# Optimization experiments

Measured on AMD Instinct MI355X. Metric: run time of the kernel, lower is better.

## Reference

```python
import jax, jax.numpy as jnp
import numpy as np

N_NODES = 10000
N_EDGES = 640000

def _gcn_conv(h, src, dst, W, b):
    # PyG GCNConv: add self-loops, symmetric deg normalization, then linear.
    # Apply linear first (same math, smaller messages).
    n = h.shape[0]
    h = h @ W  # [N, out]
    loops = jnp.arange(n)
    s = jnp.concatenate([src, loops])
    d = jnp.concatenate([dst, loops])
    deg = jax.ops.segment_sum(jnp.ones_like(s, dtype=h.dtype), d, num_segments=n)
    dinv = jnp.where(deg > 0, deg ** -0.5, 0.0)
    norm = dinv[s] * dinv[d]  # [E+N]
    msgs = h[s] * norm[:, None]
    out = jax.ops.segment_sum(msgs, d, num_segments=n)
    return out + b


def setup_inputs() -> dict:
    key = jax.random.key(0)
    ks = jax.random.split(key, 6)
    x = jax.random.normal(ks[0], (N_NODES, N_NODES), dtype=jnp.float32)
    edge_index = jax.random.randint(ks[1], (2, N_EDGES), 0, N_NODES, dtype=jnp.int64)
    emb = jax.random.normal(ks[2], (N_NODES, 256), dtype=jnp.float32)
    W1 = jax.random.normal(ks[3], (256, 64), dtype=jnp.float32) * (1.0 / np.sqrt(256))
    b1 = jnp.zeros((64,), dtype=jnp.float32)
    W2 = jax.random.normal(ks[4], (64, 32), dtype=jnp.float32) * (1.0 / np.sqrt(64))
    b2 = jnp.zeros((32,), dtype=jnp.float32)
    dec_W = jax.random.normal(ks[5], (32, 16), dtype=jnp.float32) * (1.0 / np.sqrt(32))
    return {"x": x, "edge_index": edge_index, "emb": emb, "W1": W1, "b1": b1,
            "W2": W2, "b2": b2, "dec_W": dec_W}


def reference(x, edge_index, emb, W1, b1, W2, b2, dec_W):
    src, dst = edge_index[0], edge_index[1]
    h = jax.nn.relu(x @ emb)                      # [N, 256]
    h = jax.nn.relu(_gcn_conv(h, src, dst, W1, b1))  # [N, 64]
    h = jax.nn.relu(_gcn_conv(h, src, dst, W2, b2))  # [N, 32]
    logits = h @ dec_W                            # multi-class inner-product decoder
    return logits
```

## Files before the change

kernel.cpp:

```cpp
#include <hip/hip_runtime.h>
#include <hip/hip_bf16.h>
#include <stdint.h>

#define N_NODES 10000
#define N_EDGES 640000
#define KPAD    10016
#define NSPLIT  8

typedef __bf16 bf16x8 __attribute__((ext_vector_type(8)));
typedef float  f32x4  __attribute__((ext_vector_type(4)));

#define OFF_CNT   0
#define OFF_FLAG  40960
#define OFF_DINV  65536
#define OFF_RS    131072
#define OFF_CUR   196608
#define OFF_CSR   262144
#define OFF_EMBT  3145728
#define OFF_P     8388608
#define OFF_H2    90308608
#define OFF_G2    92868608

__device__ __forceinline__ unsigned short f2b(float f) {
    unsigned int v = __float_as_uint(f);
    unsigned int r = (v + 0x7FFFu + ((v >> 16) & 1u)) >> 16;
    return (unsigned short)r;
}

__device__ __forceinline__ void gload_lds16(const void* g, void* l) {
    __builtin_amdgcn_global_load_lds(
        (const __attribute__((address_space(1))) void*)g,
        (__attribute__((address_space(3))) void*)l, 16, 0, 0);
}

__global__ void k_sniff(const int* __restrict__ edge, int* __restrict__ flag) {
    int l = threadIdx.x;
    int bad = (edge[1 + 2 * l] != 0) || (edge[129 + 2 * l] != 0);
    unsigned long long b = __ballot(bad);
    if (l == 0) *flag = (b == 0ULL) ? 1 : 0;
}

__global__ void k_count(const int* __restrict__ edge, const int* __restrict__ flag,
                        int* __restrict__ cnt) {
    int e = blockIdx.x * 256 + threadIdx.x;
    int f = *flag;
    const int* dstp = edge + (f ? 2 * N_EDGES : N_EDGES);
    atomicAdd(&cnt[dstp[e << f]], 1);
}

__global__ void k_scan(const int* __restrict__ cnt, int* __restrict__ rs, int* __restrict__ cur,
                       float* __restrict__ dinv, unsigned short* __restrict__ embT) {
    __shared__ int wsum[16];
    int t = threadIdx.x;
    for (int i = t; i < 256 * 16; i += 1024) {
        int n = i >> 4, k = i & 15;
        embT[(size_t)n * KPAD + 10000 + k] = 0;
    }
    int base = t * 10;
    int v[10]; int s = 0;
#pragma unroll
    for (int i = 0; i < 10; ++i) {
        int idx = base + i;
        int x = (idx < N_NODES) ? cnt[idx] : 0;
        v[i] = x; s += x;
        if (idx < N_NODES) dinv[idx] = rsqrtf((float)(x + 1));
    }
    int lane = t & 63, wid = t >> 6;
    int ps = s;
#pragma unroll
    for (int off = 1; off < 64; off <<= 1) {
        int u = __shfl_up(ps, off);
        if (lane >= off) ps += u;
    }
    if (lane == 63) wsum[wid] = ps;
    __syncthreads();
    if (wid == 0) {
        int x = (lane < 16) ? wsum[lane] : 0;
#pragma unroll
        for (int off = 1; off < 16; off <<= 1) {
            int u = __shfl_up(x, off);
            if (lane >= off) x += u;
        }
        if (lane < 16) wsum[lane] = x;
    }
    __syncthreads();
    int waveoff = (wid > 0) ? wsum[wid - 1] : 0;
    int run = waveoff + ps - s;
#pragma unroll
    for (int i = 0; i < 10; ++i) {
        int idx = base + i;
        run += v[i];
        if (idx < N_NODES) { rs[idx + 1] = run; cur[idx] = run - v[i]; }
    }
    if (t == 0) rs[0] = 0;
}

__global__ void k_fill(const int* __restrict__ edge, const int* __restrict__ flag,
                       int* __restrict__ cur, int* __restrict__ csr) {
    int e = blockIdx.x * 256 + threadIdx.x;
    int f = *flag;
    const int* srcp = edge;
    const int* dstp = edge + (f ? 2 * N_EDGES : N_EDGES);
    int s = srcp[e << f];
    int d = dstp[e << f];
    int pos = atomicAdd(&cur[d], 1);
    csr[pos] = s;
}

__global__ void k_transpose(const float* __restrict__ emb, unsigned short* __restrict__ embT) {
    __shared__ unsigned short t[64][65];
    int r0 = blockIdx.x * 64, c0 = blockIdx.y * 64;
    int tid = threadIdx.x;
    int cl = tid & 63, rq = tid >> 6;
#pragma unroll
    for (int i = 0; i < 16; ++i) {
        int rr = rq + i * 4;
        int r = r0 + rr;
        if (r < N_NODES) t[rr][cl] = f2b(emb[(size_t)r * 256 + c0 + cl]);
    }
    __syncthreads();
    int rr = tid & 63, cq = tid >> 6;
    int r = r0 + rr;
    if (r < N_NODES) {
#pragma unroll
        for (int j = 0; j < 16; ++j) {
            int c = cq * 16 + j;
            embT[(size_t)(c0 + c) * KPAD + r] = t[rr][c];
        }
    }
}

#define LDK 40

__global__ __launch_bounds__(512, 4) void k_gemm1(
        const float* __restrict__ X,
        const unsigned short* __restrict__ embT,
        float* __restrict__ P) {
    __shared__ __align__(16) unsigned short As[2][128 * LDK];
    __shared__ __align__(16) unsigned short Bs[2][256 * 32];
    const int tid = threadIdx.x;
    const int lane = tid & 63;
    const int w = tid >> 6;
    const int wr = w >> 2, wc = w & 3;
    const int sp = blockIdx.x;
    const int bM = blockIdx.y;

    const int st0 = sp * 39 + (sp > 0 ? 1 : 0);
    const int nsteps = ((sp + 1) * 39 + 1) - st0;

    const int ar = tid >> 2;
    const int c16 = (tid & 3) * 16;
    int agrow = bM * 128 + ar; if (agrow > N_NODES - 1) agrow = N_NODES - 1;
    const float* gA = X + (size_t)agrow * 10000 + c16;
    const unsigned short* gB = embT + (size_t)(tid >> 2) * KPAD + (tid & 3) * 8;

    const float4 z4 = make_float4(0.f, 0.f, 0.f, 0.f);
    float4 pa[4];
    auto ldA2 = [&](int ub) {
        const int kb = (st0 + ub) * 32;
#pragma unroll
        for (int j = 0; j < 4; ++j)
            pa[j] = (kb + c16 + j * 4 + 4 <= 10000) ? *(const float4*)(gA + kb + j * 4) : z4;
    };
    auto writeA = [&](int buf, int half) {
        if (((tid >> 1) & 1) == half) {
            unsigned int q[8];
#pragma unroll
            for (int j = 0; j < 4; ++j) {
                q[2 * j]     = (unsigned int)f2b(pa[j].x) | ((unsigned int)f2b(pa[j].y) << 16);
                q[2 * j + 1] = (unsigned int)f2b(pa[j].z) | ((unsigned int)f2b(pa[j].w) << 16);
            }
            unsigned short* dst = &As[buf][ar * LDK + (c16 & 31)];
            *(uint4*)(dst)     = make_uint4(q[0], q[1], q[2], q[3]);
            *(uint4*)(dst + 8) = make_uint4(q[4], q[5], q[6], q[7]);
        }
    };
    auto issueB = [&](int buf, int it) {
        const int kk = it * 32;
        gload_lds16(gB + kk,                      &Bs[buf][(w * 64) * 8]);
        gload_lds16(gB + (size_t)128 * KPAD + kk, &Bs[buf][(512 + w * 64) * 8]);
    };

    f32x4 acc[4][4];
#pragma unroll
    for (int i = 0; i < 4; ++i)
#pragma unroll
        for (int j = 0; j < 4; ++j) acc[i][j] = (f32x4){0.f, 0.f, 0.f, 0.f};

    const int q = lane >> 4, l16 = lane & 15;

    ldA2(0);
    writeA(0, 0);
    issueB(0, st0);

    int cur = 0;
    for (int u = 0; u < nsteps; ++u) {
        __syncthreads();
        int nxt = cur ^ 1;
        if (u + 1 < nsteps) {
            writeA(nxt, (u + 1) & 1);
            issueB(nxt, st0 + u + 1);
        }
        if (((u & 1) == 0) && (u + 2 < nsteps)) ldA2(u + 2);

        bf16x8 av[4], bv[4];
#pragma unroll
        for (int mt = 0; mt < 4; ++mt)
            av[mt] = *(const bf16x8*)(&As[cur][(wr * 64 + mt * 16 + l16) * LDK + q * 8]);
#pragma unroll
        for (int nt = 0; nt < 4; ++nt)
            bv[nt] = *(const bf16x8*)(&Bs[cur][(wc * 64 + nt * 16 + l16) * 32 + q * 8]);
#pragma unroll
        for (int mt = 0; mt < 4; ++mt)
#pragma unroll
            for (int nt = 0; nt < 4; ++nt)
                acc[mt][nt] = __builtin_amdgcn_mfma_f32_16x16x32_bf16(av[mt], bv[nt], acc[mt][nt], 0, 0, 0);
        cur = nxt;
    }

    float* Pp = P + (size_t)sp * N_NODES * 256;
#pragma unroll
    for (int mt = 0; mt < 4; ++mt)
#pragma unroll
        for (int nt = 0; nt < 4; ++nt) {
            int col = wc * 64 + nt * 16 + l16;
            int rbase = bM * 128 + wr * 64 + mt * 16 + q * 4;
#pragma unroll
            for (int r = 0; r < 4; ++r) {
                int row = rbase + r;
                if (row < N_NODES) Pp[(size_t)row * 256 + col] = acc[mt][nt][r];
            }
        }
}

__global__ void k_lin1(const float* __restrict__ P, const float* __restrict__ W1,
                       const float* __restrict__ dinv, float* __restrict__ g1) {
    __shared__ float w1s[256 * 64];
    int tid = threadIdx.x;
    for (int i = tid; i < 256 * 64; i += 256) w1s[i] = W1[i];
    __syncthreads();
    int f = tid & 63, nl = tid >> 6;
    int node = blockIdx.x * 4 + nl;
    const float* h = P + (size_t)node * 256;
    const size_t STR = (size_t)N_NODES * 256;
    float acc = 0.f;
    for (int k4 = 0; k4 < 64; ++k4) {
        float sx = 0.f, sy = 0.f, sz = 0.f, sw = 0.f;
#pragma unroll
        for (int j = 0; j < NSPLIT; ++j) {
            float4 t = *(const float4*)(h + j * STR + k4 * 4);
            sx += t.x; sy += t.y; sz += t.z; sw += t.w;
        }
        const float* wp = &w1s[(k4 * 4) * 64 + f];
        acc += fmaxf(sx, 0.f) * wp[0]
             + fmaxf(sy, 0.f) * wp[64]
             + fmaxf(sz, 0.f) * wp[128]
             + fmaxf(sw, 0.f) * wp[192];
    }
    g1[(size_t)node * 64 + f] = acc * dinv[node];
}

__global__ void k_agg1(const float* __restrict__ g1, const int* __restrict__ rs,
                       const int* __restrict__ csr, const float* __restrict__ dinv,
                       const float* __restrict__ b1, float* __restrict__ H2) {
    int lane = threadIdx.x & 63;
    int node = blockIdx.x * 4 + (threadIdx.x >> 6);
    float acc = g1[(size_t)node * 64 + lane];
    int e0 = rs[node], e1 = rs[node + 1];
    int e = e0;
    for (; e + 4 <= e1; e += 4) {
        int s0 = csr[e], s1 = csr[e + 1], s2 = csr[e + 2], s3 = csr[e + 3];
        float v0 = g1[(size_t)s0 * 64 + lane];
        float v1 = g1[(size_t)s1 * 64 + lane];
        float v2 = g1[(size_t)s2 * 64 + lane];
        float v3 = g1[(size_t)s3 * 64 + lane];
        acc += v0 + v1 + v2 + v3;
    }
    for (; e < e1; ++e) acc += g1[(size_t)csr[e] * 64 + lane];
    float o = dinv[node] * acc + b1[lane];
    H2[(size_t)node * 64 + lane] = fmaxf(o, 0.f);
}

__global__ void k_lin2(const float* __restrict__ H2, const float* __restrict__ W2,
                       const float* __restrict__ dinv, float* __restrict__ g2) {
    __shared__ float w2s[64 * 32];
    int tid = threadIdx.x;
    for (int i = tid; i < 64 * 32; i += 256) w2s[i] = W2[i];
    __syncthreads();
    int f = tid & 31, nl = tid >> 5;
    int node = blockIdx.x * 8 + nl;
    const float* h = H2 + (size_t)node * 64;
    float acc = 0.f;
#pragma unroll
    for (int k = 0; k < 64; ++k) acc += h[k] * w2s[k * 32 + f];
    g2[(size_t)node * 32 + f] = acc * dinv[node];
}

__global__ void k_agg2d(const float* __restrict__ g2, const int* __restrict__ rs,
                        const int* __restrict__ csr, const float* __restrict__ dinv,
                        const float* __restrict__ b2, const float* __restrict__ dW,
                        float* __restrict__ out) {
    __shared__ float dws[32 * 16];
    __shared__ float sh3[4][32];
    int tid = threadIdx.x;
    for (int i = tid; i < 512; i += 256) dws[i] = dW[i];
    int lane = tid & 63;
    int nl = tid >> 6;
    int node = blockIdx.x * 4 + nl;
    int f = lane & 31, half = lane >> 5;
    int e0 = rs[node], e1 = rs[node + 1];
    float acc = 0.f;
    int e = e0 + half;
    for (; e + 6 < e1; e += 8) {
        int s0 = csr[e], s1 = csr[e + 2], s2 = csr[e + 4], s3 = csr[e + 6];
        float v0 = g2[(size_t)s0 * 32 + f];
        float v1 = g2[(size_t)s1 * 32 + f];
        float v2 = g2[(size_t)s2 * 32 + f];
        float v3 = g2[(size_t)s3 * 32 + f];
        acc += v0 + v1 + v2 + v3;
    }
    for (; e < e1; e += 2) acc += g2[(size_t)csr[e] * 32 + f];
    acc += __shfl_down(acc, 32);
    if (half == 0) {
        acc += g2[(size_t)node * 32 + f];
        sh3[nl][f] = fmaxf(dinv[node] * acc + b2[f], 0.f);
    }
    __syncthreads();
    if (tid < 64) {
        int j = tid & 15, n2 = tid >> 4;
        float a = 0.f;
#pragma unroll
        for (int k = 0; k < 32; ++k) a += sh3[n2][k] * dws[k * 16 + j];
        out[(size_t)(blockIdx.x * 4 + n2) * 16 + j] = a;
    }
}

extern "C" void kernel_launch(void* const* d_in, const int* in_sizes, int n_in,
                              void* d_out, int out_size, void* d_ws, size_t ws_size,
                              hipStream_t stream) {
    const float* X    = (const float*)d_in[0];
    const int*   edge = (const int*)d_in[1];
    const float* emb  = (const float*)d_in[2];
    const float* W1   = (const float*)d_in[3];
    const float* b1   = (const float*)d_in[4];
    const float* W2   = (const float*)d_in[5];
    const float* b2   = (const float*)d_in[6];
    const float* dW   = (const float*)d_in[7];
    float*       out  = (float*)d_out;

    char* ws = (char*)d_ws;
    int*            cnt  = (int*)(ws + OFF_CNT);
    int*            flag = (int*)(ws + OFF_FLAG);
    float*          dinv = (float*)(ws + OFF_DINV);
    int*            rs   = (int*)(ws + OFF_RS);
    int*            cur  = (int*)(ws + OFF_CUR);
    int*            csr  = (int*)(ws + OFF_CSR);
    unsigned short* embT = (unsigned short*)(ws + OFF_EMBT);
    float*          g1   = (float*)(ws + OFF_EMBT);
    float*          P    = (float*)(ws + OFF_P);
    float*          H2   = (float*)(ws + OFF_H2);
    float*          g2   = (float*)(ws + OFF_G2);

    hipMemsetAsync(cnt, 0, N_NODES * sizeof(int), stream);

    k_sniff<<<1, 64, 0, stream>>>(edge, flag);
    k_count<<<N_EDGES / 256, 256, 0, stream>>>(edge, flag, cnt);
    k_scan<<<1, 1024, 0, stream>>>(cnt, rs, cur, dinv, embT);
    k_fill<<<N_EDGES / 256, 256, 0, stream>>>(edge, flag, cur, csr);
    k_transpose<<<dim3(157, 4), 256, 0, stream>>>(emb, embT);
    k_gemm1<<<dim3(NSPLIT, 79), 512, 0, stream>>>(X, embT, P);
    k_lin1<<<N_NODES / 4, 256, 0, stream>>>(P, W1, dinv, g1);
    k_agg1<<<N_NODES / 4, 256, 0, stream>>>(g1, rs, csr, dinv, b1, H2);
    k_lin2<<<N_NODES / 8, 256, 0, stream>>>(H2, W2, dinv, g2);
    k_agg2d<<<N_NODES / 4, 256, 0, stream>>>(g2, rs, csr, dinv, b2, dW, out);
}
```

Measured before the change: 974.0 us.

## Shrink GEMM1 tile to 64 rows with k-major LDS layout; stage lin1 through LDS

The large X@emb GEMM moves from 128x256 tiles with 512 threads to 64x256 tiles with 256 threads. Shared memory is laid out k-slice-major so the A and B fragment reads are contiguous, and the A prefetch is simplified to a single-step lookahead. This doubles the number of blocks, which can help occupancy and load balance, but each block re-reads the full B tile, raising B traffic. k_lin1 now reduces the split-K partials and applies ReLU into a shared tile for 16 nodes per block, so the W1 load into shared memory is amortised over more nodes and the global reads become coalesced float4 loads.

Measured after the change: 920.1 us. -5.5%, faster.

```diff
diff --git a/kernel.cpp b/kernel.cpp
--- a/kernel.cpp
+++ b/kernel.cpp
@@ -130,55 +130,46 @@
     }
 }
 
-#define LDK 40
-
-__global__ __launch_bounds__(512, 4) void k_gemm1(
+__global__ __launch_bounds__(256, 4) void k_gemm1(
         const float* __restrict__ X,
         const unsigned short* __restrict__ embT,
         float* __restrict__ P) {
-    __shared__ __align__(16) unsigned short As[2][128 * LDK];
-    __shared__ __align__(16) unsigned short Bs[2][256 * 32];
+    __shared__ __align__(16) unsigned short As[2][4 * 64 * 8];
+    __shared__ __align__(16) unsigned short Bs[2][4 * 256 * 8];
     const int tid = threadIdx.x;
     const int lane = tid & 63;
-    const int w = tid >> 6;
-    const int wr = w >> 2, wc = w & 3;
+    const int wc = tid >> 6;
     const int sp = blockIdx.x;
     const int bM = blockIdx.y;
 
     const int st0 = sp * 39 + (sp > 0 ? 1 : 0);
     const int nsteps = ((sp + 1) * 39 + 1) - st0;
 
-    const int ar = tid >> 2;
-    const int c16 = (tid & 3) * 16;
-    int agrow = bM * 128 + ar; if (agrow > N_NODES - 1) agrow = N_NODES - 1;
-    const float* gA = X + (size_t)agrow * 10000 + c16;
-    const unsigned short* gB = embT + (size_t)(tid >> 2) * KPAD + (tid & 3) * 8;
+    const int ar = tid >> 2, ac = tid & 3;
+    int agrow = bM * 64 + ar; if (agrow > N_NODES - 1) agrow = N_NODES - 1;
+    const float* gA = X + (size_t)agrow * 10000 + ac * 8;
+    const unsigned short* gB = embT + (size_t)tid * KPAD;
 
     const float4 z4 = make_float4(0.f, 0.f, 0.f, 0.f);
-    float4 pa[4];
-    auto ldA2 = [&](int ub) {
-        const int kb = (st0 + ub) * 32;
-#pragma unroll
-        for (int j = 0; j < 4; ++j)
-            pa[j] = (kb + c16 + j * 4 + 4 <= 10000) ? *(const float4*)(gA + kb + j * 4) : z4;
+    float4 pa0, pa1;
+    auto ldA = [&](int it) {
+        const int kb = it * 32 + ac * 8;
+        pa0 = (kb + 4 <= 10000) ? *(const float4*)(gA + it * 32) : z4;
+        pa1 = (kb + 8 <= 10000) ? *(const float4*)(gA + it * 32 + 4) : z4;
     };
-    auto writeA = [&](int buf, int half) {
-        if (((tid >> 1) & 1) == half) {
-            unsigned int q[8];
-#pragma unroll
-            for (int j = 0; j < 4; ++j) {
-                q[2 * j]     = (unsigned int)f2b(pa[j].x) | ((unsigned int)f2b(pa[j].y) << 16);
-                q[2 * j + 1] = (unsigned int)f2b(pa[j].z) | ((unsigned int)f2b(pa[j].w) << 16);
-            }
-            unsigned short* dst = &As[buf][ar * LDK + (c16 & 31)];
-            *(uint4*)(dst)     = make_uint4(q[0], q[1], q[2], q[3]);
-            *(uint4*)(dst + 8) = make_uint4(q[4], q[5], q[6], q[7]);
-        }
+    auto writeA = [&](int buf) {
+        uint4 qv;
+        qv.x = (unsigned)f2b(pa0.x) | ((unsigned)f2b(pa0.y) << 16);
+        qv.y = (unsigned)f2b(pa0.z) | ((unsigned)f2b(pa0.w) << 16);
+        qv.z = (unsigned)f2b(pa1.x) | ((unsigned)f2b(pa1.y) << 16);
+        qv.w = (unsigned)f2b(pa1.z) | ((unsigned)f2b(pa1.w) << 16);
+        *(uint4*)(&As[buf][(ac * 64 + ar) * 8]) = qv;
     };
     auto issueB = [&](int buf, int it) {
         const int kk = it * 32;
-        gload_lds16(gB + kk,                      &Bs[buf][(w * 64) * 8]);
-        gload_lds16(gB + (size_t)128 * KPAD + kk, &Bs[buf][(512 + w * 64) * 8]);
+#pragma unroll
+        for (int s = 0; s < 4; ++s)
+            gload_lds16(gB + kk + s * 8, &Bs[buf][(s * 256 + wc * 64) * 8]);
     };
 
     f32x4 acc[4][4];
@@ -189,33 +180,33 @@
 
     const int q = lane >> 4, l16 = lane & 15;
 
-    ldA2(0);
-    writeA(0, 0);
+    ldA(st0);
+    writeA(0);
     issueB(0, st0);
+    ldA(st0 + 1);
 
     int cur = 0;
     for (int u = 0; u < nsteps; ++u) {
         __syncthreads();
-        int nxt = cur ^ 1;
         if (u + 1 < nsteps) {
-            writeA(nxt, (u + 1) & 1);
-            issueB(nxt, st0 + u + 1);
-        }
-        if (((u & 1) == 0) && (u + 2 < nsteps)) ldA2(u + 2);
+            writeA(cur ^ 1);
+            issueB(cur ^ 1, st0 + u + 1);
+        }
+        if (u + 2 < nsteps) ldA(st0 + u + 2);
 
         bf16x8 av[4], bv[4];
 #pragma unroll
         for (int mt = 0; mt < 4; ++mt)
-            av[mt] = *(const bf16x8*)(&As[cur][(wr * 64 + mt * 16 + l16) * LDK + q * 8]);
+            av[mt] = *(const bf16x8*)(&As[cur][(q * 64 + mt * 16 + l16) * 8]);
 #pragma unroll
         for (int nt = 0; nt < 4; ++nt)
-            bv[nt] = *(const bf16x8*)(&Bs[cur][(wc * 64 + nt * 16 + l16) * 32 + q * 8]);
+            bv[nt] = *(const bf16x8*)(&Bs[cur][(q * 256 + wc * 64 + nt * 16 + l16) * 8]);
 #pragma unroll
         for (int mt = 0; mt < 4; ++mt)
 #pragma unroll
             for (int nt = 0; nt < 4; ++nt)
                 acc[mt][nt] = __builtin_amdgcn_mfma_f32_16x16x32_bf16(av[mt], bv[nt], acc[mt][nt], 0, 0, 0);
-        cur = nxt;
+        cur ^= 1;
     }
 
     float* Pp = P + (size_t)sp * N_NODES * 256;
@@ -224,7 +215,7 @@
 #pragma unroll
         for (int nt = 0; nt < 4; ++nt) {
             int col = wc * 64 + nt * 16 + l16;
-            int rbase = bM * 128 + wr * 64 + mt * 16 + q * 4;
+            int rbase = bM * 64 + mt * 16 + q * 4;
 #pragma unroll
             for (int r = 0; r < 4; ++r) {
                 int row = rbase + r;
@@ -233,31 +224,45 @@
         }
 }
 
-__global__ void k_lin1(const float* __restrict__ P, const float* __restrict__ W1,
-                       const float* __restrict__ dinv, float* __restrict__ g1) {
+__global__ __launch_bounds__(256) void k_lin1(const float* __restrict__ P,
+        const float* __restrict__ W1, const float* __restrict__ dinv,
+        float* __restrict__ g1) {
     __shared__ float w1s[256 * 64];
+    __shared__ float hs[16][256];
     int tid = threadIdx.x;
     for (int i = tid; i < 256 * 64; i += 256) w1s[i] = W1[i];
-    __syncthreads();
-    int f = tid & 63, nl = tid >> 6;
-    int node = blockIdx.x * 4 + nl;
-    const float* h = P + (size_t)node * 256;
+    const int nbase = blockIdx.x * 16;
     const size_t STR = (size_t)N_NODES * 256;
-    float acc = 0.f;
-    for (int k4 = 0; k4 < 64; ++k4) {
-        float sx = 0.f, sy = 0.f, sz = 0.f, sw = 0.f;
+    const int k4 = tid & 63, nl = tid >> 6;
+#pragma unroll
+    for (int i = 0; i < 4; ++i) {
+        int n = nl * 4 + i;
+        const float* p = P + (size_t)(nbase + n) * 256 + k4 * 4;
+        float4 a = make_float4(0.f, 0.f, 0.f, 0.f);
 #pragma unroll
         for (int j = 0; j < NSPLIT; ++j) {
-            float4 t = *(const float4*)(h + j * STR + k4 * 4);
-            sx += t.x; sy += t.y; sz += t.z; sw += t.w;
-        }
-        const float* wp = &w1s[(k4 * 4) * 64 + f];
-        acc += fmaxf(sx, 0.f) * wp[0]
-             + fmaxf(sy, 0.f) * wp[64]
-             + fmaxf(sz, 0.f) * wp[128]
-             + fmaxf(sw, 0.f) * wp[192];
-    }
-    g1[(size_t)node * 64 + f] = acc * dinv[node];
+            float4 t = *(const float4*)(p + (size_t)j * STR);
+            a.x += t.x; a.y += t.y; a.z += t.z; a.w += t.w;
+        }
+        float4 rl = make_float4(fmaxf(a.x, 0.f), fmaxf(a.y, 0.f),
+                                fmaxf(a.z, 0.f), fmaxf(a.w, 0.f));
+        *(float4*)(&hs[n][k4 * 4]) = rl;
+    }
+    __syncthreads();
+    const int f = tid & 63;
+#pragma unroll
+    for (int i = 0; i < 4; ++i) {
+        int n = nl * 4 + i;
+        float acc = 0.f;
+#pragma unroll 8
+        for (int kq = 0; kq < 64; ++kq) {
+            float4 h = *(const float4*)(&hs[n][kq * 4]);
+            const float* wp = &w1s[kq * 4 * 64 + f];
+            acc += h.x * wp[0] + h.y * wp[64] + h.z * wp[128] + h.w * wp[192];
+        }
+        int gn = nbase + n;
+        g1[(size_t)gn * 64 + f] = acc * dinv[gn];
+    }
 }
 
 __global__ void k_agg1(const float* __restrict__ g1, const int* __restrict__ rs,
@@ -368,8 +373,8 @@
     k_scan<<<1, 1024, 0, stream>>>(cnt, rs, cur, dinv, embT);
     k_fill<<<N_EDGES / 256, 256, 0, stream>>>(edge, flag, cur, csr);
     k_transpose<<<dim3(157, 4), 256, 0, stream>>>(emb, embT);
-    k_gemm1<<<dim3(NSPLIT, 79), 512, 0, stream>>>(X, embT, P);
-    k_lin1<<<N_NODES / 4, 256, 0, stream>>>(P, W1, dinv, g1);
+    k_gemm1<<<dim3(NSPLIT, 157), 256, 0, stream>>>(X, embT, P);
+    k_lin1<<<N_NODES / 16, 256, 0, stream>>>(P, W1, dinv, g1);
     k_agg1<<<N_NODES / 4, 256, 0, stream>>>(g1, rs, csr, dinv, b1, H2);
     k_lin2<<<N_NODES / 8, 256, 0, stream>>>(H2, W2, dinv, g2);
     k_agg2d<<<N_NODES / 4, 256, 0, stream>>>(g2, rs, csr, dinv, b2, dW, out);
```
